# Performance work log

Hardware: AMD Instinct MI355X
Metric: run time of the kernel (lower is better)

## Reference

```python
import jax, jax.numpy as jnp
import numpy as np

B = 4096
MESH = 778
NJ = 16
NBASES = 10
NPOSE = 6
PARENTS = [0, 0, 1, 2, 0, 4, 5, 0, 7, 8, 0, 10, 11, 0, 13, 14]
TIP_VERTS = [(4, 333), (8, 444), (12, 672), (16, 555), (20, 745)]


def _skew(v):
    # v: [N,3] -> [N,3,3] skew-symmetric
    x, y, z = v[:, 0], v[:, 1], v[:, 2]
    O = jnp.zeros_like(x)
    return jnp.stack([O, -z, y, z, O, -x, -y, x, O], axis=1).reshape(-1, 3, 3)


def rodrigues(r):
    # r: [N,3] axis-angle -> [N,3,3] rotation (with small-angle Taylor fallback)
    theta = jnp.sqrt(jnp.sum(r * r, axis=1))
    th_safe = jnp.maximum(theta, 1e-12)
    n = r / th_safe[:, None]
    Sn = _skew(n)
    Sr = _skew(r)
    I3 = jnp.eye(3, dtype=r.dtype)
    R = I3 + jnp.sin(theta)[:, None, None] * Sn + (1.0 - jnp.cos(theta))[:, None, None] * jnp.matmul(Sn, Sn)
    th2 = theta ** 2
    R2 = I3 + (1.0 - th2 / 6.0)[:, None, None] * Sr + (0.5 - th2 / 24.0)[:, None, None] * jnp.matmul(Sr, Sr)
    return jnp.where((theta < 1e-30)[:, None, None], R2, R)


def mano_forward(root_angles, other_angles, betas, v_template, shapedirs, posedirs,
                 J_regressor, weights, hands_components, hands_mean):
    b = root_angles.shape[0]
    dt = root_angles.dtype

    # full pose: root rotation [pi,0,0] + PCA-decoded 15 joint axis-angles
    pose_body = (hands_mean[None, :] + other_angles @ hands_components).reshape(b, NJ - 1, 3)
    root_rot = jnp.broadcast_to(jnp.array([np.pi, 0.0, 0.0], dt), (b, 1, 3))
    poses = jnp.concatenate([root_rot, pose_body], axis=1)  # [B,16,3]

    # shape blendshapes: v_shaped [B,778,3]
    v_shaped = v_template[None] + jnp.einsum('bk,mck->bmc', betas, shapedirs)

    # pose blendshapes
    R_body = rodrigues(poses[:, 1:].reshape(-1, 3))  # [B*15,3,3]
    pose_w = (R_body - jnp.eye(3, dtype=dt)).reshape(b, (NJ - 1) * 9)  # [B,135]
    v_posed = v_shaped + jnp.einsum('mcp,bp->bmc', posedirs, pose_w)

    # rest joints [B,16,3]
    J = jnp.einsum('bmc,jm->bjc', v_shaped, J_regressor)

    # per-joint rotations [B,16,3,3]
    R_all = rodrigues(poses.reshape(-1, 3)).reshape(b, NJ, 3, 3)

    def with_zeros(x):  # [B,3,4] -> [B,4,4]
        row = jnp.broadcast_to(jnp.array([0.0, 0.0, 0.0, 1.0], dt), (b, 1, 4))
        return jnp.concatenate([x, row], axis=1)

    # kinematic chain (16 joints, fixed tree)
    G = [None] * NJ
    G[0] = with_zeros(jnp.concatenate([R_all[:, 0], J[:, 0, :, None]], axis=2))
    for i in range(1, NJ):
        p = PARENTS[i]
        local = with_zeros(jnp.concatenate([R_all[:, i], (J[:, i] - J[:, p])[:, :, None]], axis=2))
        G[i] = jnp.matmul(G[p], local)
    Gs = jnp.stack(G, axis=1)  # [B,16,4,4]

    # remove rest-pose joint translation
    Jh = jnp.concatenate([J, jnp.zeros((b, NJ, 1), dt)], axis=2)[..., None]  # [B,16,4,1]
    t = jnp.matmul(Gs, Jh)  # [B,16,4,1]
    A = Gs - jnp.concatenate([jnp.zeros((b, NJ, 4, 3), dt), t], axis=-1)  # [B,16,4,4]

    # LBS skinning: T[b,p,q,m] = sum_j A[b,j,p,q] * weights[m,j]
    T = jnp.einsum('bjpq,mj->bpqm', A, weights)  # [B,4,4,778]
    rest_h = jnp.concatenate([v_posed, jnp.ones((b, MESH, 1), dt)], axis=2)  # [B,778,4]
    v = jnp.einsum('bpqm,bmq->bpm', T, rest_h)  # [B,4,778]

    # global rotation
    Rots = rodrigues(root_angles)  # [B,3,3]

    # joints: 16 chain joints + 5 fingertip vertices inserted at fixed slots
    Jtr = [Gs[:, i, :3, 3:4] for i in range(NJ)]
    for pos, vid in TIP_VERTS:
        Jtr.insert(pos, v[:, :3, vid][:, :, None])
    Jtr = jnp.concatenate(Jtr, axis=2)  # [B,3,21]

    vertices = jnp.matmul(Rots, v[:, :3, :]).transpose(0, 2, 1)  # [B,778,3]
    joint = jnp.matmul(Rots, Jtr).transpose(0, 2, 1)  # [B,21,3]
    return vertices, joint


def setup_inputs() -> dict:
    key = jax.random.key(0)
    ks = jax.random.split(key, 11)
    f32 = jnp.float32
    return {
        'root_angles': jax.random.normal(ks[0], (B, 3), f32),
        'other_angles': jax.random.normal(ks[1], (B, NPOSE), f32),
        'betas': jax.random.normal(ks[2], (B, NBASES), f32),
        'v_template': jax.random.normal(ks[3], (MESH, 3), f32) * 0.05,
        'shapedirs': jax.random.normal(ks[4], (MESH, 3, NBASES), f32) * 0.01,
        'posedirs': jax.random.normal(ks[5], (MESH, 3, (NJ - 1) * 9), f32) * 0.01,
        'J_regressor': jax.nn.softmax(jax.random.normal(ks[6], (NJ, MESH), f32), axis=1),
        'weights': jax.nn.softmax(jax.random.normal(ks[7], (MESH, NJ), f32), axis=1),
        'hands_components': jax.random.normal(ks[8], (NPOSE, (NJ - 1) * 3), f32) * 0.5,
        'hands_mean': jax.random.normal(ks[9], ((NJ - 1) * 3,), f32) * 0.1,
    }


def reference(root_angles, other_angles, betas, v_template, shapedirs, posedirs,
              J_regressor, weights, hands_components, hands_mean):
    return mano_forward(root_angles, other_angles, betas, v_template, shapedirs,
                        posedirs, J_regressor, weights, hands_components, hands_mean)
```

## Files before the change

### kernel.cpp

```cpp
#include <hip/hip_runtime.h>
#include <hip/hip_bf16.h>

#define NB 4096
#define NGRP 256
#define MESH 778
#define NPP 3136
#define JOUT (NB*MESH*3)
#define PI_F 3.14159265358979323846f

#define F_JS   0
#define F_PW   528
#define F_AF   (F_PW + 160*NB)
#define F_AH   (F_AF + 192*NB)
#define F_AL   (F_AH + 80*NB)
#define F_BTH  (F_AL + 80*NB)
#define F_BTL  (F_BTH + NPP*80)
#define F_T16H (F_BTL + NPP*80)
#define F_T16L (F_T16H + NGRP*3072)
#define WS_NEED_BYTES ((size_t)(F_T16L + NGRP*3072 + 64) * 4)

typedef __attribute__((ext_vector_type(8))) short short8;
typedef __attribute__((ext_vector_type(4))) float f32x4;

__device__ __forceinline__ unsigned short rne_bf16(float x){
  unsigned u = __float_as_uint(x);
  return (unsigned short)((u + 0x7FFFu + ((u>>16)&1u)) >> 16);
}
__device__ __forceinline__ float bf16f(unsigned short h){
  return __uint_as_float(((unsigned)h)<<16);
}

__device__ __forceinline__ void rodrigues(float x, float y, float z, float* R){
  float t2 = x*x + y*y + z*z;
  float th = sqrtf(t2);
  if (th < 1e-30f){
    float a = 1.0f - t2*(1.0f/6.0f);
    float b = 0.5f - t2*(1.0f/24.0f);
    R[0] = 1.0f + b*(x*x - t2); R[1] = -a*z + b*x*y;       R[2] = a*y + b*x*z;
    R[3] = a*z + b*x*y;         R[4] = 1.0f + b*(y*y - t2); R[5] = -a*x + b*y*z;
    R[6] = -a*y + b*x*z;        R[7] = a*x + b*y*z;        R[8] = 1.0f + b*(z*z - t2);
  } else {
    float inv = 1.0f / fmaxf(th, 1e-12f);
    float nx = x*inv, ny = y*inv, nz = z*inv;
    float s = sinf(th), c = cosf(th), ic = 1.0f - c;
    R[0] = c + ic*nx*nx;    R[1] = ic*nx*ny - s*nz; R[2] = ic*nx*nz + s*ny;
    R[3] = ic*ny*nx + s*nz; R[4] = c + ic*ny*ny;    R[5] = ic*ny*nz - s*nx;
    R[6] = ic*nz*nx - s*ny; R[7] = ic*nz*ny + s*nx; R[8] = c + ic*nz*nz;
  }
}

__global__ __launch_bounds__(256) void kJP(const float* __restrict__ vt,
    const float* __restrict__ sd, const float* __restrict__ pd,
    const float* __restrict__ jreg, float* __restrict__ ws){
  __shared__ float s_part[4];
  if (blockIdx.x < 528){
    int j = blockIdx.x / 33, combo = blockIdx.x - j*33;
    int c = combo / 11, k = combo - c*11;
    float acc = 0.f;
    for (int m = threadIdx.x; m < MESH; m += 256){
      float jr = jreg[j*MESH + m];
      float x = (k < 10) ? sd[(m*3 + c)*10 + k] : vt[m*3 + c];
      acc += jr * x;
    }
    #pragma unroll
    for (int off = 32; off; off >>= 1) acc += __shfl_down(acc, off, 64);
    int lane = threadIdx.x & 63, w = threadIdx.x >> 6;
    if (lane == 0) s_part[w] = acc;
    __syncthreads();
    if (threadIdx.x == 0)
      ws[j*33 + combo] = s_part[0]+s_part[1]+s_part[2]+s_part[3];
  } else {
    int idx = (blockIdx.x-528)*256 + threadIdx.x;
    if (idx >= NPP*160) return;
    int chunk = idx >> 9, q = idx & 511;
    int ln = q >> 3, e = q & 7;
    int tile = chunk/5, ks = chunk - tile*5;
    int c16 = ln & 15, kg = ln >> 4;
    int np = tile*16 + c16;
    int k  = ks*32 + kg*8 + e;
    int m = np >> 2, c = np & 3;
    float x = 0.f;
    if (c < 3 && m < MESH){
      int row = m*3 + c;
      if (k < 135) x = pd[(size_t)row*135 + k];
      else if (k < 145) x = sd[row*10 + (k-135)];
      else if (k == 145) x = vt[row];
    }
    ((unsigned short*)(ws + F_BTH))[idx] = rne_bf16(x);
  }
}

__global__ __launch_bounds__(256) void kB(const float* __restrict__ root,
    const float* __restrict__ other, const float* __restrict__ bet,
    const float* __restrict__ hc, const float* __restrict__ hm,
    float* __restrict__ ws, float* __restrict__ out){
  int b = blockIdx.x*256 + threadIdx.x;
  if (b >= NB) return;
  int ch = blockIdx.y;
  float* Pw = ws + F_PW;
  float* Af = ws + F_AF;

  float o[6];
  #pragma unroll
  for (int u=0;u<6;++u) o[u] = other[b*6+u];
  float bt[10];
  #pragma unroll
  for (int k=0;k<10;++k) bt[k] = bet[b*10+k];
  float Rot[9];
  rodrigues(root[b*3+0], root[b*3+1], root[b*3+2], Rot);
  float R0[9];
  rodrigues(PI_F, 0.f, 0.f, R0);
  float J0[3];
  #pragma unroll
  for (int c=0;c<3;++c){
    float a = ws[c*11 + 10];
    #pragma unroll
    for (int k=0;k<10;++k) a += bt[k]*ws[c*11 + k];
    J0[c]=a;
  }
  if (ch == 0){
    #pragma unroll
    for (int k=135;k<160;++k)
      Pw[(size_t)k*NB + b] = (k < 145) ? bt[k-135] : (k == 145 ? 1.0f : 0.f);
    float tr0[3];
    #pragma unroll
    for (int r=0;r<3;++r){
      float tr = J0[r];
      #pragma unroll
      for (int d=0;d<3;++d) tr -= R0[r*3+d]*J0[d];
      tr0[r]=tr;
    }
    #pragma unroll
    for (int r=0;r<3;++r)
      #pragma unroll
      for (int cc=0;cc<4;++cc){
        float v = 0.f;
        #pragma unroll
        for (int d=0;d<3;++d) v += Rot[r*3+d]*((cc<3)? R0[d*3+cc] : tr0[d]);
        Af[(size_t)(r*4+cc)*NB + b] = v;
      }
    int base = JOUT + b*63;
    #pragma unroll
    for (int c=0;c<3;++c)
      out[base+c] = Rot[c*3+0]*J0[0]+Rot[c*3+1]*J0[1]+Rot[c*3+2]*J0[2];
  }
  float GpR[9], Gpt[3], Jp[3];
  #pragma unroll
  for (int e=0;e<9;++e) GpR[e]=R0[e];
  #pragma unroll
  for (int c=0;c<3;++c){ Gpt[c]=J0[c]; Jp[c]=J0[c]; }
  int start = 1 + ch*3;
  #pragma unroll 1
  for (int s=0;s<3;++s){
    int i = start+s;
    int q0 = (i-1)*3;
    float rx=hm[q0], ry=hm[q0+1], rz=hm[q0+2];
    #pragma unroll
    for (int u=0;u<6;++u){
      rx += o[u]*hc[u*45+q0+0];
      ry += o[u]*hc[u*45+q0+1];
      rz += o[u]*hc[u*45+q0+2];
    }
    float Rl[9]; rodrigues(rx,ry,rz,Rl);
    #pragma unroll
    for (int e=0;e<9;++e){
      float v = (e==0||e==4||e==8) ? Rl[e]-1.f : Rl[e];
      Pw[(size_t)((i-1)*9+e)*NB + b] = v;
    }
    float Ji[3];
    #pragma unroll
    for (int c=0;c<3;++c){
      float a = ws[i*33 + c*11 + 10];
      #pragma unroll
      for (int k=0;k<10;++k) a += bt[k]*ws[i*33 + c*11 + k];
      Ji[c]=a;
    }
    float tl[3] = {Ji[0]-Jp[0], Ji[1]-Jp[1], Ji[2]-Jp[2]};
    float GR[9], Gt[3];
    #pragma unroll
    for (int r=0;r<3;++r){
      #pragma unroll
      for (int cc=0;cc<3;++cc)
        GR[r*3+cc] = GpR[r*3+0]*Rl[0*3+cc] + GpR[r*3+1]*Rl[1*3+cc] + GpR[r*3+2]*Rl[2*3+cc];
      Gt[r] = Gpt[r] + GpR[r*3+0]*tl[0] + GpR[r*3+1]*tl[1] + GpR[r*3+2]*tl[2];
    }
    float trv[3];
    #pragma unroll
    for (int r=0;r<3;++r)
      trv[r] = Gt[r] - (GR[r*3+0]*Ji[0] + GR[r*3+1]*Ji[1] + GR[r*3+2]*Ji[2]);
    #pragma unroll
    for (int r=0;r<3;++r)
      #pragma unroll
      for (int cc=0;cc<4;++cc){
        float v = 0.f;
        #pragma unroll
        for (int d=0;d<3;++d) v += Rot[r*3+d]*((cc<3)? GR[d*3+cc] : trv[d]);
        Af[(size_t)(i*12 + r*4+cc)*NB + b] = v;
      }
    int gx = i + (i>=4) + (i>=7) + (i>=10) + (i>=13);
    int base = JOUT + b*63 + gx*3;
    #pragma unroll
    for (int c=0;c<3;++c)
      out[base+c] = Rot[c*3+0]*Gt[0]+Rot[c*3+1]*Gt[1]+Rot[c*3+2]*Gt[2];
    #pragma unroll
    for (int e=0;e<9;++e) GpR[e]=GR[e];
    #pragma unroll
    for (int c=0;c<3;++c){ Gpt[c]=Gt[c]; Jp[c]=Ji[c]; }
  }
}

__global__ __launch_bounds__(256) void kT(float* __restrict__ ws){
  int idx = blockIdx.x*256 + threadIdx.x;
  const float* Pw = ws + F_PW;
  const float* Af = ws + F_AF;
  if (idx < NB*160){
    int chunk = idx >> 9, q = idx & 511;
    int ln = q >> 3, e = q & 7;
    int tile = chunk/5, ks = chunk - tile*5;
    int c16 = ln & 15, kg = ln >> 4;
    int b = tile*16 + c16;
    int k = ks*32 + kg*8 + e;
    float x = Pw[(size_t)k*NB + b];
    unsigned short h = rne_bf16(x);
    ((unsigned short*)(ws + F_AH))[idx] = h;
    ((unsigned short*)(ws + F_AL))[idx] = rne_bf16(x - bf16f(h));
  } else {
    int i2 = idx - NB*160;
    if (i2 >= NGRP*6144) return;
    int g = i2/6144, r = i2 - g*6144;
    int col = r >> 5, k = r & 31;
    int i16 = col/12, e = col - i16*12;
    int b = g*16 + i16;
    float x = (k < 16) ? Af[(size_t)(k*12+e)*NB + b] : 0.f;
    ((unsigned short*)(ws + F_T16H))[i2] = rne_bf16(x);
  }
}

__global__ __launch_bounds__(256) void kVS(const float* __restrict__ ws,
    const float* __restrict__ wgt, float* __restrict__ out){
  const unsigned short* Ah = (const unsigned short*)(ws + F_AH);
  const unsigned short* Al = (const unsigned short*)(ws + F_AL);
  const unsigned short* Bh = (const unsigned short*)(ws + F_BTH);
  const unsigned short* Th = (const unsigned short*)(ws + F_T16H);
  __shared__ unsigned short sW[2*16*40];
  __shared__ float T_lds[16*196];
  __shared__ float s_out[16*49];

  int t = threadIdx.x;
  int lane = t & 63, wv = t >> 6;
  int c16 = lane & 15, kg = lane >> 4;
  int g  = blockIdx.x;
  int b0 = g*16;

  const short8* pb_h = (const short8*)&Ah[((size_t)g*5) << 9];
  const short8* pb_l = (const short8*)&Al[((size_t)g*5) << 9];
  short8 bh_r[5], bl_r[5];
  #pragma unroll
  for (int ks=0; ks<5; ++ks){
    bh_r[ks] = pb_h[ks*64 + lane];
    bl_r[ks] = pb_l[ks*64 + lane];
  }

  #pragma unroll 1
  for (int it=0; it<2; ++it){
    int tile = blockIdx.y*2 + it;
    if (tile >= 49) break;
    int mB = tile*16;
    if (it) __syncthreads();

    { int m = t >> 4, j = t & 15;
      float wval = ((mB+m)<MESH) ? wgt[(mB+m)*16 + j] : 0.f;
      unsigned short h = rne_bf16(wval);
      sW[m*40 + j] = h;
      sW[640 + m*40 + j] = rne_bf16(wval - bf16f(h));
    }
    if (t < 128){
      int m = t >> 3, q = t & 7;
      ((unsigned*)sW)[m*20 + 8 + q] = 0u;
      ((unsigned*)sW)[320 + m*20 + 8 + q] = 0u;
    }

    short8 ath[3];
    #pragma unroll
    for (int tt=0; tt<3; ++tt){
      int col = (wv*3+tt)*16 + c16;
      ath[tt] = *(const short8*)&Th[(size_t)g*6144 + col*32 + kg*8];
    }

    int tileA = tile*4 + wv;
    const short8* pa_h = (const short8*)&Bh[((size_t)tileA*5) << 9];
    f32x4 accV = {0.f,0.f,0.f,0.f};
    #pragma unroll
    for (int ks=0; ks<5; ++ks){
      short8 ah = pa_h[ks*64 + lane];
      accV = __builtin_amdgcn_mfma_f32_16x16x32_bf16(ah, bh_r[ks], accV, 0, 0, 0);
      accV = __builtin_amdgcn_mfma_f32_16x16x32_bf16(ah, bl_r[ks], accV, 0, 0, 0);
    }
    __syncthreads();

    short8 wh = *(const short8*)&sW[c16*40 + kg*8];
    short8 wl = *(const short8*)&sW[640 + c16*40 + kg*8];
    #pragma unroll
    for (int tt=0; tt<3; ++tt){
      int col = (wv*3+tt)*16 + c16;
      f32x4 accT = {0.f,0.f,0.f,0.f};
      accT = __builtin_amdgcn_mfma_f32_16x16x32_bf16(wh, ath[tt], accT, 0, 0, 0);
      accT = __builtin_amdgcn_mfma_f32_16x16x32_bf16(wl, ath[tt], accT, 0, 0, 0);
      #pragma unroll
      for (int r=0;r<4;++r)
        T_lds[(kg*4+r)*196 + col] = accT[r];
    }
    __syncthreads();

    int ml = wv*4 + kg;
    int m  = mB + ml;
    int b  = b0 + c16;
    float4 t0 = *(const float4*)&T_lds[ml*196 + c16*12 + 0];
    float4 t1 = *(const float4*)&T_lds[ml*196 + c16*12 + 4];
    float4 t2 = *(const float4*)&T_lds[ml*196 + c16*12 + 8];
    float vx = accV[0], vy = accV[1], vz = accV[2];
    float r0 = t0.x*vx + t0.y*vy + t0.z*vz + t0.w;
    float r1 = t1.x*vx + t1.y*vy + t1.z*vz + t1.w;
    float r2 = t2.x*vx + t2.y*vy + t2.z*vz + t2.w;
    s_out[c16*49 + ml*3 + 0] = r0;
    s_out[c16*49 + ml*3 + 1] = r1;
    s_out[c16*49 + ml*3 + 2] = r2;
    if (m==333 || m==444 || m==672 || m==555 || m==745){
      int kt = (m==333)?4:(m==444)?8:(m==672)?12:(m==555)?16:20;
      int base = JOUT + b*63 + kt*3;
      out[base+0]=r0; out[base+1]=r1; out[base+2]=r2;
    }
    __syncthreads();

    for (int idx=t; idx<16*48; idx+=256){
      int i = idx/48, r = idx - i*48;
      if (mB + r/3 < MESH)
        out[(size_t)(b0+i)*(MESH*3) + mB*3 + r] = s_out[i*49 + r];
    }
  }
}

__global__ __launch_bounds__(256) void kM_fb(const float* __restrict__ root,
    const float* __restrict__ other, const float* __restrict__ bet,
    const float* __restrict__ vt, const float* __restrict__ sd,
    const float* __restrict__ pd, const float* __restrict__ wgt,
    const float* __restrict__ hc, const float* __restrict__ hm,
    const float* __restrict__ ws, float* __restrict__ out){
  __shared__ float s_pw[32*140];
  __shared__ float s_big[16*408];
  __shared__ float s_vp[32*51];
  __shared__ float s_betas[32*12];
  __shared__ float s_sd[16*30];
  __shared__ float s_vt[48];
  __shared__ float s_w[256];
  __shared__ float s_rot[32*12];
  __shared__ float s_oth[32*6];
  __shared__ float s_js[528];

  int t = threadIdx.x;
  int m0 = blockIdx.x*16;
  int b0 = blockIdx.y*32;

  for (int idx=t; idx<16*408; idx+=256){
    int m = idx/408, r = idx - m*408;
    int c = r/136, p = r - c*136;
    float v = 0.f;
    if (p < 135 && (m0+m) < MESH) v = pd[((size_t)(m0+m)*3+c)*135 + p];
    s_big[m*408 + c*136 + p] = v;
  }
  for (int idx=t; idx<32*10; idx+=256){
    int i = idx/10, k = idx - i*10;
    s_betas[i*12+k] = bet[(b0+i)*10+k];
  }
  for (int idx=t; idx<16*30; idx+=256){
    int m = idx/30, r = idx - m*30;
    s_sd[m*30+r] = ((m0+m)<MESH) ? sd[(m0+m)*30 + r] : 0.f;
  }
  for (int idx=t; idx<48; idx+=256){
    int m = idx/3;
    s_vt[idx] = ((m0+m)<MESH) ? vt[m0*3 + idx] : 0.f;
  }
  for (int idx=t; idx<256; idx+=256){
    int m = idx/16;
    s_w[idx] = ((m0+m)<MESH) ? wgt[m0*16 + idx] : 0.f;
  }
  for (int idx=t; idx<192; idx+=256) s_oth[idx] = other[(size_t)b0*6 + idx];
  for (int idx=t; idx<528; idx+=256) s_js[idx] = ws[idx];
  __syncthreads();

  for (int task=t; task<512; task+=256){
    if (task < 480){
      int b = task/15, jj = task - b*15;
      int q0 = jj*3;
      float rx=hm[q0], ry=hm[q0+1], rz=hm[q0+2];
      #pragma unroll
      for (int u=0;u<6;++u){
        float o = s_oth[b*6+u];
        rx += o*hc[u*45+q0+0];
        ry += o*hc[u*45+q0+1];
        rz += o*hc[u*45+q0+2];
      }
      float Rl[9]; rodrigues(rx,ry,rz,Rl);
      float* pw = &s_pw[b*140 + jj*9];
      pw[0]=Rl[0]-1.f; pw[1]=Rl[1];     pw[2]=Rl[2];
      pw[3]=Rl[3];     pw[4]=Rl[4]-1.f; pw[5]=Rl[5];
      pw[6]=Rl[6];     pw[7]=Rl[7];     pw[8]=Rl[8]-1.f;
    } else {
      int b = task-480;
      float Rr[9];
      rodrigues(root[(b0+b)*3+0], root[(b0+b)*3+1], root[(b0+b)*3+2], Rr);
      #pragma unroll
      for (int e=0;e<9;++e) s_rot[b*12+e] = Rr[e];
      s_pw[b*140 + 135] = 0.f;
    }
  }
  __syncthreads();

  int bl = t & 31, mg = t >> 5;
  float acc[2][3];
  #pragma unroll
  for (int mi=0; mi<2; ++mi){
    int ml = mg*2+mi;
    #pragma unroll
    for (int c=0; c<3; ++c){
      float a = s_vt[ml*3+c];
      #pragma unroll
      for (int k=0;k<10;++k) a += s_betas[bl*12+k]*s_sd[ml*30+c*10+k];
      acc[mi][c]=a;
    }
  }
  const float4* pwv = reinterpret_cast<const float4*>(&s_pw[bl*140]);
  #pragma unroll 2
  for (int pq=0; pq<34; ++pq){
    float4 w = pwv[pq];
    #pragma unroll
    for (int mi=0; mi<2; ++mi){
      int ml = mg*2+mi;
      #pragma unroll
      for (int c=0;c<3;++c){
        float4 d = *reinterpret_cast<const float4*>(&s_big[ml*408 + c*136 + pq*4]);
        acc[mi][c] += w.x*d.x + w.y*d.y + w.z*d.z + w.w*d.w;
      }
    }
  }
  #pragma unroll
  for (int mi=0;mi<2;++mi){
    int ml=mg*2+mi;
    #pragma unroll
    for (int c=0;c<3;++c) s_vp[bl*51+ml*3+c] = acc[mi][c];
  }
  __syncthreads();

  if (t < 160){
    int b = t/5, ch = t - b*5;
    int gb = b0 + b;
    float bt_[10];
    #pragma unroll
    for (int k=0;k<10;++k) bt_[k] = s_betas[b*12+k];
    float R0[9]; rodrigues(PI_F, 0.f, 0.f, R0);
    float J0[3];
    #pragma unroll
    for (int c=0;c<3;++c){
      float a = s_js[c*11 + 10];
      #pragma unroll
      for (int k=0;k<10;++k) a += bt_[k]*s_js[c*11 + k];
      J0[c]=a;
    }
    float Rot[9];
    #pragma unroll
    for (int e=0;e<9;++e) Rot[e] = s_rot[b*12+e];
    if (ch == 0){
      #pragma unroll
      for (int r=0;r<3;++r){
        float tr = J0[r];
        #pragma unroll
        for (int d=0;d<3;++d) tr -= R0[r*3+d]*J0[d];
        s_big[(r*4+0)*33 + b] = R0[r*3+0];
        s_big[(r*4+1)*33 + b] = R0[r*3+1];
        s_big[(r*4+2)*33 + b] = R0[r*3+2];
        s_big[(r*4+3)*33 + b] = tr;
      }
      if (blockIdx.x == 0){
        int base = JOUT + gb*63;
        #pragma unroll
        for (int c=0;c<3;++c)
          out[base+c] = Rot[c*3+0]*J0[0]+Rot[c*3+1]*J0[1]+Rot[c*3+2]*J0[2];
      }
    }
    float GpR[9], Gpt[3], Jp[3];
    #pragma unroll
    for (int e=0;e<9;++e) GpR[e]=R0[e];
    #pragma unroll
    for (int c=0;c<3;++c){ Gpt[c]=J0[c]; Jp[c]=J0[c]; }
    int start = 1 + ch*3;
    #pragma unroll 1
    for (int s=0;s<3;++s){
      int i = start+s;
      float Rl[9];
      #pragma unroll
      for (int e=0;e<9;++e){
        float v = s_pw[b*140 + (i-1)*9 + e];
        Rl[e] = (e==0||e==4||e==8) ? v+1.f : v;
      }
      float Ji[3];
      #pragma unroll
      for (int c=0;c<3;++c){
        float a = s_js[i*33 + c*11 + 10];
        #pragma unroll
        for (int k=0;k<10;++k) a += bt_[k]*s_js[i*33 + c*11 + k];
        Ji[c]=a;
      }
      float tl[3] = {Ji[0]-Jp[0], Ji[1]-Jp[1], Ji[2]-Jp[2]};
      float GR[9], Gt[3];
      #pragma unroll
      for (int r=0;r<3;++r){
        #pragma unroll
        for (int cc=0;cc<3;++cc)
          GR[r*3+cc] = GpR[r*3+0]*Rl[0*3+cc] + GpR[r*3+1]*Rl[1*3+cc] + GpR[r*3+2]*Rl[2*3+cc];
        Gt[r] = Gpt[r] + GpR[r*3+0]*tl[0] + GpR[r*3+1]*tl[1] + GpR[r*3+2]*tl[2];
      }
      #pragma unroll
      for (int r=0;r<3;++r){
        float tr = Gt[r] - (GR[r*3+0]*Ji[0] + GR[r*3+1]*Ji[1] + GR[r*3+2]*Ji[2]);
        s_big[(i*12 + r*4+0)*33 + b] = GR[r*3+0];
        s_big[(i*12 + r*4+1)*33 + b] = GR[r*3+1];
        s_big[(i*12 + r*4+2)*33 + b] = GR[r*3+2];
        s_big[(i*12 + r*4+3)*33 + b] = tr;
      }
      if (blockIdx.x == 0){
        int gx = i + (i>=4) + (i>=7) + (i>=10) + (i>=13);
        int base = JOUT + gb*63 + gx*3;
        #pragma unroll
        for (int c=0;c<3;++c)
          out[base+c] = Rot[c*3+0]*Gt[0]+Rot[c*3+1]*Gt[1]+Rot[c*3+2]*Gt[2];
      }
      #pragma unroll
      for (int e=0;e<9;++e) GpR[e]=GR[e];
      #pragma unroll
      for (int c=0;c<3;++c){ Gpt[c]=Gt[c]; Jp[c]=Ji[c]; }
    }
  }
  __syncthreads();

  #pragma unroll
  for (int mi=0;mi<2;++mi){
    int ml = mg*2+mi; int m = m0+ml;
    float T[12];
    #pragma unroll
    for (int e=0;e<12;++e) T[e]=0.f;
    #pragma unroll
    for (int j=0;j<16;++j){
      float wj = s_w[ml*16+j];
      #pragma unroll
      for (int e=0;e<12;++e) T[e] += wj * s_big[(j*12+e)*33 + bl];
    }
    float vx = s_vp[bl*51+ml*3+0];
    float vy = s_vp[bl*51+ml*3+1];
    float vz = s_vp[bl*51+ml*3+2];
    float v0 = T[0]*vx+T[1]*vy+T[2]*vz+T[3];
    float v1 = T[4]*vx+T[5]*vy+T[6]*vz+T[7];
    float v2 = T[8]*vx+T[9]*vy+T[10]*vz+T[11];
    float r0 = s_rot[bl*12+0]*v0 + s_rot[bl*12+1]*v1 + s_rot[bl*12+2]*v2;
    float r1 = s_rot[bl*12+3]*v0 + s_rot[bl*12+4]*v1 + s_rot[bl*12+5]*v2;
    float r2 = s_rot[bl*12+6]*v0 + s_rot[bl*12+7]*v1 + s_rot[bl*12+8]*v2;
    s_pw[bl*49 + ml*3 + 0] = r0;
    s_pw[bl*49 + ml*3 + 1] = r1;
    s_pw[bl*49 + ml*3 + 2] = r2;
    if (m==333 || m==444 || m==672 || m==555 || m==745){
      int kt = (m==333)?4:(m==444)?8:(m==672)?12:(m==555)?16:20;
      int base = JOUT + (b0+bl)*63 + kt*3;
      out[base+0]=r0; out[base+1]=r1; out[base+2]=r2;
    }
  }
  __syncthreads();

  for (int idx=t; idx<32*48; idx+=256){
    int i = idx/48, r = idx - i*48;
    if (m0 + r/3 < MESH)
      out[(size_t)(b0+i)*(MESH*3) + m0*3 + r] = s_pw[i*49 + r];
  }
}

extern "C" void kernel_launch(void* const* d_in, const int* in_sizes, int n_in,
                              void* d_out, int out_size, void* d_ws, size_t ws_size,
                              hipStream_t stream) {
  const float* root  = (const float*)d_in[0];
  const float* other = (const float*)d_in[1];
  const float* bet   = (const float*)d_in[2];
  const float* vt    = (const float*)d_in[3];
  const float* sd    = (const float*)d_in[4];
  const float* pdirs = (const float*)d_in[5];
  const float* jreg  = (const float*)d_in[6];
  const float* wgt   = (const float*)d_in[7];
  const float* hc    = (const float*)d_in[8];
  const float* hm    = (const float*)d_in[9];
  float* ws = (float*)d_ws;
  float* out = (float*)d_out;

  if (ws_size >= WS_NEED_BYTES){
    kJP<<<dim3(528 + (NPP*160+255)/256), dim3(256), 0, stream>>>(vt, sd, pdirs, jreg, ws);
    kB<<<dim3(16, 5), dim3(256), 0, stream>>>(root, other, bet, hc, hm, ws, out);
    kT<<<dim3((NB*160 + NGRP*6144 + 255)/256), dim3(256), 0, stream>>>(ws);
    kVS<<<dim3(NGRP, 25), dim3(256), 0, stream>>>(ws, wgt, out);
  } else {
    kJP<<<dim3(528), dim3(256), 0, stream>>>(vt, sd, pdirs, jreg, ws);
    kM_fb<<<dim3(49, 128), dim3(256), 0, stream>>>(root, other, bet, vt, sd, pdirs,
                                                   wgt, hc, hm, ws, out);
  }
}
```

Measured before the change: 60.64 us.

## Double-buffer skinning weights and process four mesh tiles per block

Each kVS block now handles four mesh tiles instead of two, so the grid in y shrinks from 25 to 13. The per-group T16 fragments are loaded once, outside the tile loop. Skinning weights for the next tile are converted into a second LDS buffer while the current tile is computed. This amortizes the per-block register loads of A and T over more tiles and removes one barrier per iteration, at the cost of fewer blocks for latency hiding. The end-of-loop barrier ordering for reusing the alternate buffer must still hold.

```diff
diff --git a/kernel.cpp b/kernel.cpp
--- a/kernel.cpp
+++ b/kernel.cpp
@@ -242,7 +242,7 @@
   const unsigned short* Al = (const unsigned short*)(ws + F_AL);
   const unsigned short* Bh = (const unsigned short*)(ws + F_BTH);
   const unsigned short* Th = (const unsigned short*)(ws + F_T16H);
-  __shared__ unsigned short sW[2*16*40];
+  __shared__ unsigned short sW[2][1280];
   __shared__ float T_lds[16*196];
   __shared__ float s_out[16*49];
 
@@ -251,6 +251,7 @@
   int c16 = lane & 15, kg = lane >> 4;
   int g  = blockIdx.x;
   int b0 = g*16;
+  int tile0 = blockIdx.y*4;
 
   const short8* pb_h = (const short8*)&Ah[((size_t)g*5) << 9];
   const short8* pb_l = (const short8*)&Al[((size_t)g*5) << 9];
@@ -260,31 +261,42 @@
     bh_r[ks] = pb_h[ks*64 + lane];
     bl_r[ks] = pb_l[ks*64 + lane];
   }
+  short8 ath[3];
+  #pragma unroll
+  for (int tt=0; tt<3; ++tt){
+    int col = (wv*3+tt)*16 + c16;
+    ath[tt] = *(const short8*)&Th[(size_t)g*6144 + col*32 + kg*8];
+  }
+
+  if (t < 128){
+    int m = t >> 3, q = t & 7;
+    ((unsigned*)sW[0])[m*20 + 8 + q] = 0u;
+    ((unsigned*)sW[0])[320 + m*20 + 8 + q] = 0u;
+    ((unsigned*)sW[1])[m*20 + 8 + q] = 0u;
+    ((unsigned*)sW[1])[320 + m*20 + 8 + q] = 0u;
+  }
+  { int m = t >> 4, j = t & 15;
+    int mB = tile0*16;
+    float wval = ((mB+m)<MESH) ? wgt[(mB+m)*16 + j] : 0.f;
+    unsigned short h = rne_bf16(wval);
+    sW[0][m*40 + j] = h;
+    sW[0][640 + m*40 + j] = rne_bf16(wval - bf16f(h));
+  }
 
   #pragma unroll 1
-  for (int it=0; it<2; ++it){
-    int tile = blockIdx.y*2 + it;
+  for (int it=0; it<4; ++it){
+    int tile = tile0 + it;
     if (tile >= 49) break;
     int mB = tile*16;
-    if (it) __syncthreads();
-
-    { int m = t >> 4, j = t & 15;
-      float wval = ((mB+m)<MESH) ? wgt[(mB+m)*16 + j] : 0.f;
+    int cur = it & 1;
+
+    if (it < 3 && tile+1 < 49){
+      int m = t >> 4, j = t & 15;
+      int mBn = (tile+1)*16;
+      float wval = ((mBn+m)<MESH) ? wgt[(mBn+m)*16 + j] : 0.f;
       unsigned short h = rne_bf16(wval);
-      sW[m*40 + j] = h;
-      sW[640 + m*40 + j] = rne_bf16(wval - bf16f(h));
-    }
-    if (t < 128){
-      int m = t >> 3, q = t & 7;
-      ((unsigned*)sW)[m*20 + 8 + q] = 0u;
-      ((unsigned*)sW)[320 + m*20 + 8 + q] = 0u;
-    }
-
-    short8 ath[3];
-    #pragma unroll
-    for (int tt=0; tt<3; ++tt){
-      int col = (wv*3+tt)*16 + c16;
-      ath[tt] = *(const short8*)&Th[(size_t)g*6144 + col*32 + kg*8];
+      sW[cur^1][m*40 + j] = h;
+      sW[cur^1][640 + m*40 + j] = rne_bf16(wval - bf16f(h));
     }
 
     int tileA = tile*4 + wv;
@@ -298,8 +310,8 @@
     }
     __syncthreads();
 
-    short8 wh = *(const short8*)&sW[c16*40 + kg*8];
-    short8 wl = *(const short8*)&sW[640 + c16*40 + kg*8];
+    short8 wh = *(const short8*)&sW[cur][c16*40 + kg*8];
+    short8 wl = *(const short8*)&sW[cur][640 + c16*40 + kg*8];
     #pragma unroll
     for (int tt=0; tt<3; ++tt){
       int col = (wv*3+tt)*16 + c16;
@@ -601,7 +613,7 @@
     kJP<<<dim3(528 + (NPP*160+255)/256), dim3(256), 0, stream>>>(vt, sd, pdirs, jreg, ws);
     kB<<<dim3(16, 5), dim3(256), 0, stream>>>(root, other, bet, hc, hm, ws, out);
     kT<<<dim3((NB*160 + NGRP*6144 + 255)/256), dim3(256), 0, stream>>>(ws);
-    kVS<<<dim3(NGRP, 25), dim3(256), 0, stream>>>(ws, wgt, out);
+    kVS<<<dim3(NGRP, 13), dim3(256), 0, stream>>>(ws, wgt, out);
   } else {
     kJP<<<dim3(528), dim3(256), 0, stream>>>(vt, sd, pdirs, jreg, ws);
     kM_fb<<<dim3(49, 128), dim3(256), 0, stream>>>(root, other, bet, vt, sd, pdirs,
```

New measurement: 54.56 us (median of 2 runs). 1.11x faster.
